# Performance work log

Measured on AMD Instinct MI355X. Metric: run time of the kernel, lower is better.

Reference implementation:

```python
import jax, jax.numpy as jnp
import numpy as np
from jax import lax

C, H, O = 95, 128, 4
B, T = 256, 1000
EPS = 1e-5


def setup_inputs() -> dict:
    key = jax.random.key(0)
    ks = jax.random.split(key, 8)
    x = jax.random.normal(ks[0], (B, T, C), dtype=jnp.float32)
    # BatchNorm1d params (eval mode: running stats)
    gamma = jnp.ones((C,), jnp.float32)
    beta = jnp.zeros((C,), jnp.float32)
    running_mean = jnp.zeros((C,), jnp.float32)
    running_var = jnp.ones((C,), jnp.float32)
    # LSTM params, torch gate order (i, f, g, o), init U(-1/sqrt(H), 1/sqrt(H))
    s = 1.0 / np.sqrt(H)
    W_ih = jax.random.uniform(ks[1], (4 * H, C), jnp.float32, -s, s)
    W_hh = jax.random.uniform(ks[2], (4 * H, H), jnp.float32, -s, s)
    b_ih = jax.random.uniform(ks[3], (4 * H,), jnp.float32, -s, s)
    b_hh = jax.random.uniform(ks[4], (4 * H,), jnp.float32, -s, s)
    # Final linear
    sf = 1.0 / np.sqrt(H)
    fc_w = jax.random.uniform(ks[5], (O, H), jnp.float32, -sf, sf)
    fc_b = jax.random.uniform(ks[6], (O,), jnp.float32, -sf, sf)
    return {"x": x, "gamma": gamma, "beta": beta,
            "running_mean": running_mean, "running_var": running_var,
            "W_ih": W_ih, "W_hh": W_hh, "b_ih": b_ih, "b_hh": b_hh,
            "fc_w": fc_w, "fc_b": fc_b}


def reference(x, gamma, beta, running_mean, running_var,
              W_ih, W_hh, b_ih, b_hh, fc_w, fc_b):
    # BatchNorm1d over channel dim (last axis of [B,T,C]), eval semantics
    inv = gamma * lax.rsqrt(running_var + EPS)
    xn = (x - running_mean) * inv + beta  # [B,T,C]
    # Precompute input contribution to all gates for every timestep
    xW = jnp.einsum('btc,gc->btg', xn, W_ih) + (b_ih + b_hh)  # [B,T,4H]

    def step(carry, xw_t):
        h, c = carry  # [B,H] each
        gates = xw_t + h @ W_hh.T  # [B,4H]
        i, f, g, o = jnp.split(gates, 4, axis=-1)
        i = jax.nn.sigmoid(i)
        f = jax.nn.sigmoid(f)
        g = jnp.tanh(g)
        o = jax.nn.sigmoid(o)
        c = f * c + i * g
        h = o * jnp.tanh(c)
        return (h, c), None

    h0 = jnp.zeros((x.shape[0], H), x.dtype)
    c0 = jnp.zeros((x.shape[0], H), x.dtype)
    (h_T, _), _ = lax.scan(step, (h0, c0), jnp.swapaxes(xW, 0, 1))  # scan over time
    return h_T @ fc_w.T + fc_b  # [B,O]
```

## Files before the change

kernel.cpp:

```cpp
#include <hip/hip_runtime.h>
#include <cstdint>

constexpr int Cc = 95;
constexpr int Hh = 128;
constexpr int G  = 512;
constexpr int Bb = 256;
constexpr int Tt = 1000;
#define EPSBN 1e-5f

typedef _Float16 half8  __attribute__((ext_vector_type(8)));
typedef float floatx4 __attribute__((ext_vector_type(4)));
typedef float float4u __attribute__((ext_vector_type(4), aligned(4)));
typedef float float2u __attribute__((ext_vector_type(2), aligned(4)));

__device__ __forceinline__ unsigned pku(float a, float b) {
  return __builtin_bit_cast(unsigned, __builtin_amdgcn_cvt_pkrtz(a, b));
}
__device__ __forceinline__ float fsigm(float y) {
  y = fminf(30.f, fmaxf(-30.f, y));
  float e = __expf(-y);
  return __fdividef(1.f, 1.f + e);
}
__device__ __forceinline__ float ftanh2(float x) {
  float y = fminf(30.f, fmaxf(-30.f, 2.f * x));
  float e = __expf(y);
  return __fdividef(e - 1.f, e + 1.f);
}

__global__ __launch_bounds__(512)
void k0_prep(const float* __restrict__ gamma, const float* __restrict__ beta,
             const float* __restrict__ rmean, const float* __restrict__ rvar,
             const float* __restrict__ W_ih, const float* __restrict__ b_ih,
             const float* __restrict__ b_hh, float* __restrict__ biasp,
             _Float16* __restrict__ Wp) {
  __shared__ float scl[Cc], sft[Cc];
  const int t = threadIdx.x;
  if (t < Cc) {
    float s = gamma[t] * rsqrtf(rvar[t] + EPSBN);
    scl[t] = s;
    sft[t] = beta[t] - rmean[t] * s;
  }
  __syncthreads();
  float acc = b_ih[t] + b_hh[t];
  const float* wr = W_ih + (size_t)t * Cc;
  for (int c = 0; c < Cc; ++c) {
    float w = wr[c];
    acc = fmaf(sft[c], w, acc);
    Wp[t * 96 + c] = (_Float16)(w * scl[c]);
  }
  Wp[t * 96 + 95] = (_Float16)0.f;
  biasp[t] = acc;
}

template <int TC>
__global__ __launch_bounds__(512)
void k1_mfma(const float* __restrict__ x, const _Float16* __restrict__ Wp,
             const float* __restrict__ biasp, float* __restrict__ xw, int t0) {
  const int tid = threadIdx.x;
  const int wave = tid >> 6, lane = tid & 63;
  const int wm = wave >> 2, wn = wave & 3;
  const int row0 = blockIdx.x * 64 + wm * 32;
  const int nb0 = wn * 128;
  const int l15 = lane & 15, lg = lane >> 4;

  uint4 afr[2][3];
#pragma unroll
  for (int mt = 0; mt < 2; ++mt) {
    int m = row0 + mt * 16 + l15;
    int b = m / TC, tl = m - b * TC;
    const float* xr = x + ((size_t)b * Tt + t0 + tl) * Cc;
#pragma unroll
    for (int kk = 0; kk < 3; ++kk) {
      int k = kk * 32 + lg * 8;
      float4u p0 = *reinterpret_cast<const float4u*>(xr + k);
      float e4, e5, e6, e7;
      if (k == 88) {
        float2u q = *reinterpret_cast<const float2u*>(xr + 92);
        e4 = q[0]; e5 = q[1]; e6 = xr[94]; e7 = 0.f;
      } else {
        float4u p1 = *reinterpret_cast<const float4u*>(xr + k + 4);
        e4 = p1[0]; e5 = p1[1]; e6 = p1[2]; e7 = p1[3];
      }
      afr[mt][kk] = make_uint4(pku(p0[0], p0[1]), pku(p0[2], p0[3]),
                               pku(e4, e5), pku(e6, e7));
    }
  }

  floatx4 acc[2][8] = {};
#pragma unroll
  for (int kk = 0; kk < 3; ++kk)
#pragma unroll
    for (int nt = 0; nt < 8; ++nt) {
      const _Float16* wrow = Wp + (size_t)(nb0 + nt * 16 + l15) * 96 + lg * 8;
      uint4 bfr = *reinterpret_cast<const uint4*>(wrow + kk * 32);
      half8 bv = __builtin_bit_cast(half8, bfr);
      acc[0][nt] = __builtin_amdgcn_mfma_f32_16x16x32_f16(
          __builtin_bit_cast(half8, afr[0][kk]), bv, acc[0][nt], 0, 0, 0);
      acc[1][nt] = __builtin_amdgcn_mfma_f32_16x16x32_f16(
          __builtin_bit_cast(half8, afr[1][kk]), bv, acc[1][nt], 0, 0, 0);
    }

#pragma unroll
  for (int nt = 0; nt < 8; ++nt) {
    int n = nb0 + nt * 16 + l15;
    float bias = biasp[n];
#pragma unroll
    for (int mt = 0; mt < 2; ++mt) {
      int rbase = row0 + mt * 16 + lg * 4;
#pragma unroll
      for (int r = 0; r < 4; ++r)
        xw[(size_t)(rbase + r) * G + n] = acc[mt][nt][r] + bias;
    }
  }
}

template <int TC>
__global__ __launch_bounds__(256, 1)
void k2_lstm(const float* __restrict__ xw, const float* __restrict__ W_hh,
             float* __restrict__ hstate, float* __restrict__ cstate,
             const float* __restrict__ fc_w, const float* __restrict__ fc_b,
             float* __restrict__ out, int t0) {
  __shared__ __align__(16) _Float16 h2[2][Hh];
  __shared__ float h32[Hh];

  const int b = blockIdx.x;
  const int tid = threadIdx.x;
  const int w = tid >> 6, lane = tid & 63;
  const int l15 = lane & 15, lg = lane >> 4;
  const int hh = l15 & 1, rr = (l15 >> 1) & 3;
  const int u = 32 * w + 16 * hh + 4 * lg + rr;
  const bool owner = (l15 < 8);

  uint4 afr[8][4];
#pragma unroll
  for (int q = 0; q < 4; ++q)
#pragma unroll
    for (int h2i = 0; h2i < 2; ++h2i) {
      const float* wr =
          W_hh + (size_t)(q * 128 + 32 * w + 16 * h2i + l15) * Hh + 8 * lg;
#pragma unroll
      for (int kc = 0; kc < 4; ++kc) {
        float4u p0 = *reinterpret_cast<const float4u*>(wr + 32 * kc);
        float4u p1 = *reinterpret_cast<const float4u*>(wr + 32 * kc + 4);
        afr[2 * q + h2i][kc] = make_uint4(pku(p0[0], p0[1]), pku(p0[2], p0[3]),
                                          pku(p1[0], p1[1]), pku(p1[2], p1[3]));
      }
    }

  float creg = 0.f, hreg = 0.f;
  if (t0 == 0) {
    if (owner) h2[0][u] = (_Float16)0.f;
  } else {
    creg = cstate[b * Hh + u];
    hreg = hstate[b * Hh + u];
    if (owner) h2[0][u] = (_Float16)hreg;
  }
  __syncthreads();

  const float* xwb = xw + (size_t)b * TC * G;

  float pi[4], pf[4], pg[4], po[4];
#pragma unroll
  for (int i = 0; i < 4; ++i) {
    if (i < TC) {
      const float* xp = xwb + (size_t)i * G;
      pi[i] = xp[0 * 128 + u]; pf[i] = xp[1 * 128 + u];
      pg[i] = xp[2 * 128 + u]; po[i] = xp[3 * 128 + u];
    } else {
      pi[i] = pf[i] = pg[i] = po[i] = 0.f;
    }
  }

#define K2_STEP(TL, SL)                                                        \
  {                                                                            \
    const int tl_ = (TL);                                                      \
    const int rb_ = tl_ & 1;                                                   \
    float ci = pi[SL], cf = pf[SL], cg = pg[SL], co = po[SL];                  \
    if (tl_ + 4 < TC) {                                                        \
      const float* xp_ = xwb + (size_t)(tl_ + 4) * G;                          \
      pi[SL] = xp_[0 * 128 + u]; pf[SL] = xp_[1 * 128 + u];                    \
      pg[SL] = xp_[2 * 128 + u]; po[SL] = xp_[3 * 128 + u];                    \
    }                                                                          \
    uint4 bfr[4];                                                              \
    _Pragma("unroll") for (int kc = 0; kc < 4; ++kc)                           \
        bfr[kc] = *reinterpret_cast<const uint4*>(&h2[rb_][32 * kc + 8 * lg]); \
    floatx4 acc[8] = {};                                                       \
    _Pragma("unroll") for (int kc = 0; kc < 4; ++kc)                           \
        _Pragma("unroll") for (int t_ = 0; t_ < 8; ++t_)                       \
            acc[t_] = __builtin_amdgcn_mfma_f32_16x16x32_f16(                  \
                __builtin_bit_cast(half8, afr[t_][kc]),                        \
                __builtin_bit_cast(half8, bfr[kc]), acc[t_], 0, 0, 0);         \
    float gq[4];                                                               \
    _Pragma("unroll") for (int q_ = 0; q_ < 4; ++q_) {                         \
      float e0 = hh ? acc[2 * q_ + 1][0] : acc[2 * q_][0];                     \
      float e1 = hh ? acc[2 * q_ + 1][1] : acc[2 * q_][1];                     \
      float e2 = hh ? acc[2 * q_ + 1][2] : acc[2 * q_][2];                     \
      float e3 = hh ? acc[2 * q_ + 1][3] : acc[2 * q_][3];                     \
      float lo = (rr & 1) ? e1 : e0;                                           \
      float hi = (rr & 1) ? e3 : e2;                                           \
      gq[q_] = (rr & 2) ? hi : lo;                                             \
    }                                                                          \
    float i_ = fsigm(gq[0] + ci);                                              \
    float f_ = fsigm(gq[1] + cf);                                              \
    float g_ = ftanh2(gq[2] + cg);                                             \
    float o_ = fsigm(gq[3] + co);                                              \
    creg = fmaf(f_, creg, i_ * g_);                                            \
    hreg = o_ * ftanh2(creg);                                                  \
    if (owner) h2[rb_ ^ 1][u] = (_Float16)hreg;                                \
    asm volatile("s_waitcnt lgkmcnt(0)" ::: "memory");                         \
    __builtin_amdgcn_s_barrier();                                              \
    __builtin_amdgcn_sched_barrier(0);                                         \
  }

  int tl = 0;
  for (; tl + 4 <= TC; tl += 4) {
    K2_STEP(tl + 0, 0)
    K2_STEP(tl + 1, 1)
    K2_STEP(tl + 2, 2)
    K2_STEP(tl + 3, 3)
  }
  if constexpr ((TC & 3) >= 1) K2_STEP(TC & ~3, 0)
  if constexpr ((TC & 3) >= 2) K2_STEP((TC & ~3) + 1, 1)
  if constexpr ((TC & 3) >= 3) K2_STEP((TC & ~3) + 2, 2)
#undef K2_STEP

  if (owner) {
    hstate[b * Hh + u] = hreg;
    cstate[b * Hh + u] = creg;
    h32[u] = hreg;
  }
  __syncthreads();

  if (t0 + TC == Tt && tid < 4) {
    float s = fc_b[tid];
    for (int jj = 0; jj < Hh; ++jj) s = fmaf(h32[jj], fc_w[tid * Hh + jj], s);
    out[b * 4 + tid] = s;
  }
}

template <int TC>
static void run_chunks(const float* x, const float* gamma, const float* beta,
                       const float* rmean, const float* rvar,
                       const float* W_ih, const float* W_hh,
                       const float* b_ih, const float* b_hh,
                       const float* fc_w, const float* fc_b, float* out,
                       void* d_ws, hipStream_t stream) {
  char* ws = reinterpret_cast<char*>(d_ws);
  float* xwp  = reinterpret_cast<float*>(ws);
  size_t off  = (size_t)Bb * TC * G * 4;
  float* hst  = reinterpret_cast<float*>(ws + off);  off += (size_t)Bb * Hh * 4;
  float* cst  = reinterpret_cast<float*>(ws + off);  off += (size_t)Bb * Hh * 4;
  float* bia  = reinterpret_cast<float*>(ws + off);  off += 512 * 4;
  off = (off + 15) & ~(size_t)15;
  _Float16* Wp = reinterpret_cast<_Float16*>(ws + off);

  k0_prep<<<dim3(1), dim3(512), 0, stream>>>(gamma, beta, rmean, rvar, W_ih,
                                             b_ih, b_hh, bia, Wp);
  for (int t0 = 0; t0 < Tt; t0 += TC) {
    k1_mfma<TC><<<dim3(Bb * TC / 64), dim3(512), 0, stream>>>(x, Wp, bia, xwp,
                                                              t0);
    k2_lstm<TC><<<dim3(Bb), dim3(256), 0, stream>>>(xwp, W_hh, hst, cst, fc_w,
                                                    fc_b, out, t0);
  }
}

extern "C" void kernel_launch(void* const* d_in, const int* in_sizes, int n_in,
                              void* d_out, int out_size, void* d_ws,
                              size_t ws_size, hipStream_t stream) {
  const float* x     = (const float*)d_in[0];
  const float* gamma = (const float*)d_in[1];
  const float* beta  = (const float*)d_in[2];
  const float* rmean = (const float*)d_in[3];
  const float* rvar  = (const float*)d_in[4];
  const float* W_ih  = (const float*)d_in[5];
  const float* W_hh  = (const float*)d_in[6];
  const float* b_ih  = (const float*)d_in[7];
  const float* b_hh  = (const float*)d_in[8];
  const float* fc_w  = (const float*)d_in[9];
  const float* fc_b  = (const float*)d_in[10];
  float* out = (float*)d_out;

  auto need = [](int tc) {
    return (size_t)Bb * tc * G * 4 + 2 * (size_t)Bb * Hh * 4 + 512 * 4 + 16 +
           (size_t)512 * 96 * 2;
  };

  if (ws_size >= need(250)) {
    run_chunks<250>(x, gamma, beta, rmean, rvar, W_ih, W_hh, b_ih, b_hh, fc_w,
                    fc_b, out, d_ws, stream);
  } else if (ws_size >= need(125)) {
    run_chunks<125>(x, gamma, beta, rmean, rvar, W_ih, W_hh, b_ih, b_hh, fc_w,
                    fc_b, out, d_ws, stream);
  } else if (ws_size >= need(50)) {
    run_chunks<50>(x, gamma, beta, rmean, rvar, W_ih, W_hh, b_ih, b_hh, fc_w,
                   fc_b, out, d_ws, stream);
  } else {
    run_chunks<10>(x, gamma, beta, rmean, rvar, W_ih, W_hh, b_ih, b_hh, fc_w,
                   fc_b, out, d_ws, stream);
  }
}
```

Baseline: 841.0 us.

## Fuse input projection into persistent LSTM kernel with double-buffered chunk overlap

Replaces the per-chunk pair of GEMM and recurrence launches with a single persistent kernel per batch row. The kernel computes the next chunk's input-gate projection with MFMA, interleaved into the recurrence steps of the current chunk, and writes it into a second xw buffer. It also pre-converts x to padded fp16, moves to 8 waves per block with one unit per lane group, stores gates interleaved so one float4 load fetches all four, and drops some activation clamps. In return each recurrence step carries extra work and register pressure, and the workspace size check is gone.

```diff
diff --git a/kernel.cpp b/kernel.cpp
--- a/kernel.cpp
+++ b/kernel.cpp
@@ -6,24 +6,28 @@
 constexpr int G  = 512;
 constexpr int Bb = 256;
 constexpr int Tt = 1000;
+constexpr int TC = 125;
+constexpr int NCH = 8;
 #define EPSBN 1e-5f
 
 typedef _Float16 half8  __attribute__((ext_vector_type(8)));
 typedef float floatx4 __attribute__((ext_vector_type(4)));
 typedef float float4u __attribute__((ext_vector_type(4), aligned(4)));
-typedef float float2u __attribute__((ext_vector_type(2), aligned(4)));
 
 __device__ __forceinline__ unsigned pku(float a, float b) {
   return __builtin_bit_cast(unsigned, __builtin_amdgcn_cvt_pkrtz(a, b));
 }
+__device__ __forceinline__ floatx4 mfma16(uint4 a, uint4 b, floatx4 c) {
+  return __builtin_amdgcn_mfma_f32_16x16x32_f16(
+      __builtin_bit_cast(half8, a), __builtin_bit_cast(half8, b), c, 0, 0, 0);
+}
 __device__ __forceinline__ float fsigm(float y) {
-  y = fminf(30.f, fmaxf(-30.f, y));
   float e = __expf(-y);
   return __fdividef(1.f, 1.f + e);
 }
 __device__ __forceinline__ float ftanh2(float x) {
-  float y = fminf(30.f, fmaxf(-30.f, 2.f * x));
-  float e = __expf(y);
+  float yy = fminf(60.f, 2.f * x);
+  float e = __expf(yy);
   return __fdividef(e - 1.f, e + 1.f);
 }
 
@@ -52,158 +56,145 @@
   biasp[t] = acc;
 }
 
-template <int TC>
-__global__ __launch_bounds__(512)
-void k1_mfma(const float* __restrict__ x, const _Float16* __restrict__ Wp,
-             const float* __restrict__ biasp, float* __restrict__ xw, int t0) {
-  const int tid = threadIdx.x;
-  const int wave = tid >> 6, lane = tid & 63;
-  const int wm = wave >> 2, wn = wave & 3;
-  const int row0 = blockIdx.x * 64 + wm * 32;
-  const int nb0 = wn * 128;
-  const int l15 = lane & 15, lg = lane >> 4;
-
-  uint4 afr[2][3];
-#pragma unroll
-  for (int mt = 0; mt < 2; ++mt) {
-    int m = row0 + mt * 16 + l15;
-    int b = m / TC, tl = m - b * TC;
-    const float* xr = x + ((size_t)b * Tt + t0 + tl) * Cc;
-#pragma unroll
-    for (int kk = 0; kk < 3; ++kk) {
-      int k = kk * 32 + lg * 8;
-      float4u p0 = *reinterpret_cast<const float4u*>(xr + k);
-      float e4, e5, e6, e7;
-      if (k == 88) {
-        float2u q = *reinterpret_cast<const float2u*>(xr + 92);
-        e4 = q[0]; e5 = q[1]; e6 = xr[94]; e7 = 0.f;
-      } else {
-        float4u p1 = *reinterpret_cast<const float4u*>(xr + k + 4);
-        e4 = p1[0]; e5 = p1[1]; e6 = p1[2]; e7 = p1[3];
-      }
-      afr[mt][kk] = make_uint4(pku(p0[0], p0[1]), pku(p0[2], p0[3]),
-                               pku(e4, e5), pku(e6, e7));
-    }
-  }
-
-  floatx4 acc[2][8] = {};
-#pragma unroll
-  for (int kk = 0; kk < 3; ++kk)
-#pragma unroll
-    for (int nt = 0; nt < 8; ++nt) {
-      const _Float16* wrow = Wp + (size_t)(nb0 + nt * 16 + l15) * 96 + lg * 8;
-      uint4 bfr = *reinterpret_cast<const uint4*>(wrow + kk * 32);
-      half8 bv = __builtin_bit_cast(half8, bfr);
-      acc[0][nt] = __builtin_amdgcn_mfma_f32_16x16x32_f16(
-          __builtin_bit_cast(half8, afr[0][kk]), bv, acc[0][nt], 0, 0, 0);
-      acc[1][nt] = __builtin_amdgcn_mfma_f32_16x16x32_f16(
-          __builtin_bit_cast(half8, afr[1][kk]), bv, acc[1][nt], 0, 0, 0);
-    }
-
-#pragma unroll
-  for (int nt = 0; nt < 8; ++nt) {
-    int n = nb0 + nt * 16 + l15;
-    float bias = biasp[n];
-#pragma unroll
-    for (int mt = 0; mt < 2; ++mt) {
-      int rbase = row0 + mt * 16 + lg * 4;
-#pragma unroll
-      for (int r = 0; r < 4; ++r)
-        xw[(size_t)(rbase + r) * G + n] = acc[mt][nt][r] + bias;
-    }
-  }
-}
-
-template <int TC>
-__global__ __launch_bounds__(256, 1)
-void k2_lstm(const float* __restrict__ xw, const float* __restrict__ W_hh,
-             float* __restrict__ hstate, float* __restrict__ cstate,
+__global__ __launch_bounds__(256)
+void k0_xh(const float* __restrict__ x, _Float16* __restrict__ xh) {
+  const size_t N = (size_t)Bb * Tt * 96;
+  for (size_t i = (size_t)blockIdx.x * 256 + threadIdx.x; i < N;
+       i += (size_t)gridDim.x * 256) {
+    size_t row = i / 96;
+    int c = (int)(i - row * 96);
+    float v = (c < Cc) ? x[row * Cc + c] : 0.f;
+    xh[i] = (_Float16)v;
+  }
+}
+
+__global__ __attribute__((amdgpu_flat_work_group_size(512, 512)))
+__attribute__((amdgpu_waves_per_eu(2, 2)))
+void k2_mega(const _Float16* __restrict__ xh, const _Float16* __restrict__ Wp,
+             const float* __restrict__ biasp, const float* __restrict__ W_hh,
              const float* __restrict__ fc_w, const float* __restrict__ fc_b,
-             float* __restrict__ out, int t0) {
+             float* __restrict__ out, float* __restrict__ xw0,
+             float* __restrict__ xw1) {
   __shared__ __align__(16) _Float16 h2[2][Hh];
   __shared__ float h32[Hh];
 
   const int b = blockIdx.x;
   const int tid = threadIdx.x;
-  const int w = tid >> 6, lane = tid & 63;
+  const int w8 = tid >> 6, lane = tid & 63;
   const int l15 = lane & 15, lg = lane >> 4;
-  const int hh = l15 & 1, rr = (l15 >> 1) & 3;
-  const int u = 32 * w + 16 * hh + 4 * lg + rr;
-  const bool owner = (l15 < 8);
-
-  uint4 afr[8][4];
-#pragma unroll
-  for (int q = 0; q < 4; ++q)
-#pragma unroll
-    for (int h2i = 0; h2i < 2; ++h2i) {
-      const float* wr =
-          W_hh + (size_t)(q * 128 + 32 * w + 16 * h2i + l15) * Hh + 8 * lg;
-#pragma unroll
-      for (int kc = 0; kc < 4; ++kc) {
-        float4u p0 = *reinterpret_cast<const float4u*>(wr + 32 * kc);
-        float4u p1 = *reinterpret_cast<const float4u*>(wr + 32 * kc + 4);
-        afr[2 * q + h2i][kc] = make_uint4(pku(p0[0], p0[1]), pku(p0[2], p0[3]),
-                                          pku(p1[0], p1[1]), pku(p1[2], p1[3]));
-      }
-    }
+  const int rr = l15 & 3;
+  const int u = 16 * w8 + 4 * lg + rr;
+  const bool owner = (l15 < 4);
+
+  uint4 afr[4][4];
+#pragma unroll
+  for (int q = 0; q < 4; ++q) {
+    const float* wr = W_hh + (size_t)(q * 128 + 16 * w8 + l15) * Hh + 8 * lg;
+#pragma unroll
+    for (int kc = 0; kc < 4; ++kc) {
+      float4u p0 = *reinterpret_cast<const float4u*>(wr + 32 * kc);
+      float4u p1 = *reinterpret_cast<const float4u*>(wr + 32 * kc + 4);
+      afr[q][kc] = make_uint4(pku(p0[0], p0[1]), pku(p0[2], p0[3]),
+                              pku(p1[0], p1[1]), pku(p1[2], p1[3]));
+    }
+  }
+
+  const int qcol = w8 >> 1;
+  float biasg[4];
+#pragma unroll
+  for (int ct = 0; ct < 4; ++ct) biasg[ct] = biasp[64 * w8 + 16 * ct + l15];
+
+  uint4 Ac[3], Bp[3];
+
+#define G_ISSUE_A(RT, TB)                                                      \
+  {                                                                            \
+    const _Float16* xa =                                                       \
+        xh + ((size_t)b * Tt + (TB) + 16 * (RT) + l15) * 96 + 8 * lg;          \
+    Ac[0] = *reinterpret_cast<const uint4*>(xa);                               \
+    Ac[1] = *reinterpret_cast<const uint4*>(xa + 32);                          \
+    Ac[2] = *reinterpret_cast<const uint4*>(xa + 64);                          \
+  }
+#define G_ISSUE_B(CT)                                                          \
+  {                                                                            \
+    const _Float16* wb =                                                       \
+        Wp + (size_t)(64 * w8 + 16 * (CT) + l15) * 96 + 8 * lg;                \
+    Bp[0] = *reinterpret_cast<const uint4*>(wb);                               \
+    Bp[1] = *reinterpret_cast<const uint4*>(wb + 32);                          \
+    Bp[2] = *reinterpret_cast<const uint4*>(wb + 64);                          \
+  }
+#define G_EXEC(RT, CT, BUFN)                                                   \
+  {                                                                            \
+    floatx4 ag = {0.f, 0.f, 0.f, 0.f};                                         \
+    ag = mfma16(Ac[0], Bp[0], ag);                                             \
+    ag = mfma16(Ac[1], Bp[1], ag);                                             \
+    ag = mfma16(Ac[2], Bp[2], ag);                                             \
+    int ucol = (64 * w8 + 16 * (CT) + l15) & 127;                              \
+    float bs = biasg[CT];                                                      \
+    _Pragma("unroll") for (int r_ = 0; r_ < 4; ++r_) {                         \
+      int m_ = 16 * (RT) + 4 * lg + r_;                                        \
+      if (m_ < TC)                                                             \
+        (BUFN)[((size_t)b * TC + m_) * G + ucol * 4 + qcol] = ag[r_] + bs;     \
+    }                                                                          \
+  }
+
+  for (int rt = 0; rt < 8; ++rt) {
+    G_ISSUE_A(rt, 0)
+#pragma unroll
+    for (int ct = 0; ct < 4; ++ct) {
+      G_ISSUE_B(ct)
+      G_EXEC(rt, ct, xw0)
+    }
+  }
+  asm volatile("s_waitcnt vmcnt(0)" ::: "memory");
+  __syncthreads();
 
   float creg = 0.f, hreg = 0.f;
-  if (t0 == 0) {
-    if (owner) h2[0][u] = (_Float16)0.f;
-  } else {
-    creg = cstate[b * Hh + u];
-    hreg = hstate[b * Hh + u];
-    if (owner) h2[0][u] = (_Float16)hreg;
-  }
-  __syncthreads();
-
-  const float* xwb = xw + (size_t)b * TC * G;
-
-  float pi[4], pf[4], pg[4], po[4];
-#pragma unroll
-  for (int i = 0; i < 4; ++i) {
-    if (i < TC) {
-      const float* xp = xwb + (size_t)i * G;
-      pi[i] = xp[0 * 128 + u]; pf[i] = xp[1 * 128 + u];
-      pg[i] = xp[2 * 128 + u]; po[i] = xp[3 * 128 + u];
-    } else {
-      pi[i] = pf[i] = pg[i] = po[i] = 0.f;
-    }
-  }
+  if (owner) h2[0][u] = (_Float16)0.f;
+  __syncthreads();
+
+  const float* bc = xw0;
+  float* bn = xw1;
+
+  for (int c = 0; c < NCH; ++c) {
+    const bool dog = (c < NCH - 1);
+    const int tnext = (c + 1) * TC;
+    const float* xrb = bc + (size_t)b * TC * G + 4 * u;
+
+    float4u rg[4];
+#pragma unroll
+    for (int i = 0; i < 4; ++i)
+      rg[i] = *reinterpret_cast<const float4u*>(xrb + (size_t)i * G);
 
 #define K2_STEP(TL, SL)                                                        \
   {                                                                            \
     const int tl_ = (TL);                                                      \
     const int rb_ = tl_ & 1;                                                   \
-    float ci = pi[SL], cf = pf[SL], cg = pg[SL], co = po[SL];                  \
-    if (tl_ + 4 < TC) {                                                        \
-      const float* xp_ = xwb + (size_t)(tl_ + 4) * G;                          \
-      pi[SL] = xp_[0 * 128 + u]; pf[SL] = xp_[1 * 128 + u];                    \
-      pg[SL] = xp_[2 * 128 + u]; po[SL] = xp_[3 * 128 + u];                    \
+    float4u cg4 = rg[SL];                                                      \
+    if (tl_ + 4 < TC)                                                          \
+      rg[SL] = *reinterpret_cast<const float4u*>(xrb + (size_t)(tl_ + 4) * G); \
+    const int p_ = tl_ >> 2;                                                   \
+    if (dog && (tl_ & 3) == 0) {                                               \
+      if ((p_ & 3) == 0) G_ISSUE_A(p_ >> 2, tnext)                             \
+      G_ISSUE_B(p_ & 3)                                                        \
     }                                                                          \
     uint4 bfr[4];                                                              \
     _Pragma("unroll") for (int kc = 0; kc < 4; ++kc)                           \
         bfr[kc] = *reinterpret_cast<const uint4*>(&h2[rb_][32 * kc + 8 * lg]); \
-    floatx4 acc[8] = {};                                                       \
+    floatx4 acc[4] = {};                                                       \
     _Pragma("unroll") for (int kc = 0; kc < 4; ++kc)                           \
-        _Pragma("unroll") for (int t_ = 0; t_ < 8; ++t_)                       \
-            acc[t_] = __builtin_amdgcn_mfma_f32_16x16x32_f16(                  \
-                __builtin_bit_cast(half8, afr[t_][kc]),                        \
-                __builtin_bit_cast(half8, bfr[kc]), acc[t_], 0, 0, 0);         \
+        _Pragma("unroll") for (int q_ = 0; q_ < 4; ++q_)                       \
+            acc[q_] = mfma16(afr[q_][kc], bfr[kc], acc[q_]);                   \
+    if (dog && (tl_ & 3) == 1) G_EXEC(p_ >> 2, p_ & 3, bn)                     \
     float gq[4];                                                               \
     _Pragma("unroll") for (int q_ = 0; q_ < 4; ++q_) {                         \
-      float e0 = hh ? acc[2 * q_ + 1][0] : acc[2 * q_][0];                     \
-      float e1 = hh ? acc[2 * q_ + 1][1] : acc[2 * q_][1];                     \
-      float e2 = hh ? acc[2 * q_ + 1][2] : acc[2 * q_][2];                     \
-      float e3 = hh ? acc[2 * q_ + 1][3] : acc[2 * q_][3];                     \
-      float lo = (rr & 1) ? e1 : e0;                                           \
-      float hi = (rr & 1) ? e3 : e2;                                           \
+      float lo = (rr & 1) ? acc[q_][1] : acc[q_][0];                           \
+      float hi = (rr & 1) ? acc[q_][3] : acc[q_][2];                           \
       gq[q_] = (rr & 2) ? hi : lo;                                             \
     }                                                                          \
-    float i_ = fsigm(gq[0] + ci);                                              \
-    float f_ = fsigm(gq[1] + cf);                                              \
-    float g_ = ftanh2(gq[2] + cg);                                             \
-    float o_ = fsigm(gq[3] + co);                                              \
+    float i_ = fsigm(gq[0] + cg4[0]);                                          \
+    float f_ = fsigm(gq[1] + cg4[1]);                                          \
+    float g_ = ftanh2(gq[2] + cg4[2]);                                         \
+    float o_ = fsigm(gq[3] + cg4[3]);                                          \
     creg = fmaf(f_, creg, i_ * g_);                                            \
     hreg = o_ * ftanh2(creg);                                                  \
     if (owner) h2[rb_ ^ 1][u] = (_Float16)hreg;                                \
@@ -212,56 +203,37 @@
     __builtin_amdgcn_sched_barrier(0);                                         \
   }
 
-  int tl = 0;
-  for (; tl + 4 <= TC; tl += 4) {
-    K2_STEP(tl + 0, 0)
-    K2_STEP(tl + 1, 1)
-    K2_STEP(tl + 2, 2)
-    K2_STEP(tl + 3, 3)
-  }
-  if constexpr ((TC & 3) >= 1) K2_STEP(TC & ~3, 0)
-  if constexpr ((TC & 3) >= 2) K2_STEP((TC & ~3) + 1, 1)
-  if constexpr ((TC & 3) >= 3) K2_STEP((TC & ~3) + 2, 2)
+    int tl = 0;
+    for (; tl + 4 <= TC; tl += 4) {
+      K2_STEP(tl + 0, 0)
+      K2_STEP(tl + 1, 1)
+      K2_STEP(tl + 2, 2)
+      K2_STEP(tl + 3, 3)
+    }
+    K2_STEP(124, 0)
 #undef K2_STEP
 
-  if (owner) {
-    hstate[b * Hh + u] = hreg;
-    cstate[b * Hh + u] = creg;
-    h32[u] = hreg;
-  }
-  __syncthreads();
-
-  if (t0 + TC == Tt && tid < 4) {
+    if (dog) {
+      G_EXEC(7, 3, bn)
+      asm volatile("s_waitcnt vmcnt(0)" ::: "memory");
+    }
+    __syncthreads();
+    const float* tmp = bc;
+    bc = bn;
+    bn = const_cast<float*>(tmp);
+  }
+
+  if (owner) h32[u] = hreg;
+  __syncthreads();
+
+  if (tid < 4) {
     float s = fc_b[tid];
     for (int jj = 0; jj < Hh; ++jj) s = fmaf(h32[jj], fc_w[tid * Hh + jj], s);
     out[b * 4 + tid] = s;
   }
-}
-
-template <int TC>
-static void run_chunks(const float* x, const float* gamma, const float* beta,
-                       const float* rmean, const float* rvar,
-                       const float* W_ih, const float* W_hh,
-                       const float* b_ih, const float* b_hh,
-                       const float* fc_w, const float* fc_b, float* out,
-                       void* d_ws, hipStream_t stream) {
-  char* ws = reinterpret_cast<char*>(d_ws);
-  float* xwp  = reinterpret_cast<float*>(ws);
-  size_t off  = (size_t)Bb * TC * G * 4;
-  float* hst  = reinterpret_cast<float*>(ws + off);  off += (size_t)Bb * Hh * 4;
-  float* cst  = reinterpret_cast<float*>(ws + off);  off += (size_t)Bb * Hh * 4;
-  float* bia  = reinterpret_cast<float*>(ws + off);  off += 512 * 4;
-  off = (off + 15) & ~(size_t)15;
-  _Float16* Wp = reinterpret_cast<_Float16*>(ws + off);
-
-  k0_prep<<<dim3(1), dim3(512), 0, stream>>>(gamma, beta, rmean, rvar, W_ih,
-                                             b_ih, b_hh, bia, Wp);
-  for (int t0 = 0; t0 < Tt; t0 += TC) {
-    k1_mfma<TC><<<dim3(Bb * TC / 64), dim3(512), 0, stream>>>(x, Wp, bia, xwp,
-                                                              t0);
-    k2_lstm<TC><<<dim3(Bb), dim3(256), 0, stream>>>(xwp, W_hh, hst, cst, fc_w,
-                                                    fc_b, out, t0);
-  }
+#undef G_ISSUE_A
+#undef G_ISSUE_B
+#undef G_EXEC
 }
 
 extern "C" void kernel_launch(void* const* d_in, const int* in_sizes, int n_in,
@@ -280,22 +252,17 @@
   const float* fc_b  = (const float*)d_in[10];
   float* out = (float*)d_out;
 
-  auto need = [](int tc) {
-    return (size_t)Bb * tc * G * 4 + 2 * (size_t)Bb * Hh * 4 + 512 * 4 + 16 +
-           (size_t)512 * 96 * 2;
-  };
-
-  if (ws_size >= need(250)) {
-    run_chunks<250>(x, gamma, beta, rmean, rvar, W_ih, W_hh, b_ih, b_hh, fc_w,
-                    fc_b, out, d_ws, stream);
-  } else if (ws_size >= need(125)) {
-    run_chunks<125>(x, gamma, beta, rmean, rvar, W_ih, W_hh, b_ih, b_hh, fc_w,
-                    fc_b, out, d_ws, stream);
-  } else if (ws_size >= need(50)) {
-    run_chunks<50>(x, gamma, beta, rmean, rvar, W_ih, W_hh, b_ih, b_hh, fc_w,
-                   fc_b, out, d_ws, stream);
-  } else {
-    run_chunks<10>(x, gamma, beta, rmean, rvar, W_ih, W_hh, b_ih, b_hh, fc_w,
-                   fc_b, out, d_ws, stream);
-  }
-}
+  char* ws = reinterpret_cast<char*>(d_ws);
+  const size_t S1 = (size_t)Bb * TC * G * 4;
+  float* xw0 = reinterpret_cast<float*>(ws);
+  float* xw1 = reinterpret_cast<float*>(ws + S1);
+  float* bia = reinterpret_cast<float*>(ws + 2 * S1);
+  _Float16* Wp = reinterpret_cast<_Float16*>(ws + 2 * S1 + 2048);
+  _Float16* xh = reinterpret_cast<_Float16*>(ws + 2 * S1 + 2048 + 98304);
+
+  k0_prep<<<dim3(1), dim3(512), 0, stream>>>(gamma, beta, rmean, rvar, W_ih,
+                                             b_ih, b_hh, bia, Wp);
+  k0_xh<<<dim3(2048), dim3(256), 0, stream>>>(x, xh);
+  k2_mega<<<dim3(Bb), dim3(512), 0, stream>>>(xh, Wp, bia, W_hh, fc_w, fc_b,
+                                              out, xw0, xw1);
+}
```

After: 851.6 us. About the same (+1.3%).

## Pack two batch rows per LSTM block with 512-thread workgroups

Applied to the files above, without the earlier changes.

The recurrent LSTM kernel now handles two batch elements per workgroup, using 8 waves split into two sub-groups, each with its own double-buffered h state in LDS. The grid is halved to 128 blocks of 512 threads, and the final FC computes outputs for both rows. The aim is to put two independent recurrences on each CU so their latency-bound MFMA and transcendental chains can interleave on the SIMDs. In exchange, half the CUs on a 256-CU part sit idle, every per-step barrier now spans 8 waves, and register pressure is capped by the waves-per-EU hint.

```diff
diff --git a/kernel.cpp b/kernel.cpp
--- a/kernel.cpp
+++ b/kernel.cpp
@@ -115,20 +115,23 @@
 }
 
 template <int TC>
-__global__ __launch_bounds__(256, 1)
+__global__ __attribute__((amdgpu_flat_work_group_size(512, 512)))
+__attribute__((amdgpu_waves_per_eu(2, 2)))
 void k2_lstm(const float* __restrict__ xw, const float* __restrict__ W_hh,
              float* __restrict__ hstate, float* __restrict__ cstate,
              const float* __restrict__ fc_w, const float* __restrict__ fc_b,
              float* __restrict__ out, int t0) {
-  __shared__ __align__(16) _Float16 h2[2][Hh];
-  __shared__ float h32[Hh];
-
-  const int b = blockIdx.x;
+  __shared__ __align__(16) _Float16 h2[2][2][Hh];
+  __shared__ float h32[2][Hh];
+
   const int tid = threadIdx.x;
-  const int w = tid >> 6, lane = tid & 63;
+  const int wave = tid >> 6, lane = tid & 63;
+  const int sub = wave >> 2;
+  const int w = wave & 3;
   const int l15 = lane & 15, lg = lane >> 4;
   const int hh = l15 & 1, rr = (l15 >> 1) & 3;
   const int u = 32 * w + 16 * hh + 4 * lg + rr;
+  const int b = blockIdx.x * 2 + sub;
   const bool owner = (l15 < 8);
 
   uint4 afr[8][4];
@@ -149,11 +152,11 @@
 
   float creg = 0.f, hreg = 0.f;
   if (t0 == 0) {
-    if (owner) h2[0][u] = (_Float16)0.f;
+    if (owner) h2[sub][0][u] = (_Float16)0.f;
   } else {
     creg = cstate[b * Hh + u];
     hreg = hstate[b * Hh + u];
-    if (owner) h2[0][u] = (_Float16)hreg;
+    if (owner) h2[sub][0][u] = (_Float16)hreg;
   }
   __syncthreads();
 
@@ -182,8 +185,8 @@
       pg[SL] = xp_[2 * 128 + u]; po[SL] = xp_[3 * 128 + u];                    \
     }                                                                          \
     uint4 bfr[4];                                                              \
-    _Pragma("unroll") for (int kc = 0; kc < 4; ++kc)                           \
-        bfr[kc] = *reinterpret_cast<const uint4*>(&h2[rb_][32 * kc + 8 * lg]); \
+    _Pragma("unroll") for (int kc = 0; kc < 4; ++kc) bfr[kc] =                 \
+        *reinterpret_cast<const uint4*>(&h2[sub][rb_][32 * kc + 8 * lg]);      \
     floatx4 acc[8] = {};                                                       \
     _Pragma("unroll") for (int kc = 0; kc < 4; ++kc)                           \
         _Pragma("unroll") for (int t_ = 0; t_ < 8; ++t_)                       \
@@ -206,7 +209,7 @@
     float o_ = fsigm(gq[3] + co);                                              \
     creg = fmaf(f_, creg, i_ * g_);                                            \
     hreg = o_ * ftanh2(creg);                                                  \
-    if (owner) h2[rb_ ^ 1][u] = (_Float16)hreg;                                \
+    if (owner) h2[sub][rb_ ^ 1][u] = (_Float16)hreg;                           \
     asm volatile("s_waitcnt lgkmcnt(0)" ::: "memory");                         \
     __builtin_amdgcn_s_barrier();                                              \
     __builtin_amdgcn_sched_barrier(0);                                         \
@@ -227,14 +230,17 @@
   if (owner) {
     hstate[b * Hh + u] = hreg;
     cstate[b * Hh + u] = creg;
-    h32[u] = hreg;
+    h32[sub][u] = hreg;
   }
   __syncthreads();
 
-  if (t0 + TC == Tt && tid < 4) {
-    float s = fc_b[tid];
-    for (int jj = 0; jj < Hh; ++jj) s = fmaf(h32[jj], fc_w[tid * Hh + jj], s);
-    out[b * 4 + tid] = s;
+  if (t0 + TC == Tt && tid < 8) {
+    int s2 = tid >> 2, g = tid & 3;
+    int bb = blockIdx.x * 2 + s2;
+    float s = fc_b[g];
+    for (int jj = 0; jj < Hh; ++jj)
+      s = fmaf(h32[s2][jj], fc_w[g * Hh + jj], s);
+    out[bb * 4 + g] = s;
   }
 }
 
@@ -259,8 +265,8 @@
   for (int t0 = 0; t0 < Tt; t0 += TC) {
     k1_mfma<TC><<<dim3(Bb * TC / 64), dim3(512), 0, stream>>>(x, Wp, bia, xwp,
                                                               t0);
-    k2_lstm<TC><<<dim3(Bb), dim3(256), 0, stream>>>(xwp, W_hh, hst, cst, fc_w,
-                                                    fc_b, out, t0);
+    k2_lstm<TC><<<dim3(Bb / 2), dim3(512), 0, stream>>>(xwp, W_hh, hst, cst,
+                                                        fc_w, fc_b, out, t0);
   }
 }
 
```

After: 1.153 ms. 1.37x slower.
